# Performance work log

Hardware: AMD Instinct MI355X
Metric: run time of the kernel (lower is better)

The kernel has to match this reference:

```python
import jax, jax.numpy as jnp
import numpy as np

B, N_P, N_S = 64, 50, 200
N_NODES = N_P * N_S          # 10000 nodes per graph (jobs x ops)
N_CAND = N_S + 1             # 201 candidates
INPUT_DIM, HIDDEN = 3, 64
NODE_DIM = 2 * HIDDEN        # h_nodes feature dim (=> actor in = 6*HIDDEN)
POOL_DIM = 4 * HIDDEN        # h_pooled dim (mean || max pooling)
H_ACTOR, H_CRITIC = 256, 256


def setup_inputs() -> dict:
    key = jax.random.key(0)
    ks = jax.random.split(key, 16)
    p = lambda k, sh: jax.random.normal(k, sh, jnp.float32) * 0.02
    x = jax.random.normal(ks[0], (B, N_NODES, INPUT_DIM), jnp.float32)
    candidate = jax.random.randint(ks[1], (B, N_CAND), 0, N_NODES)
    mask = jax.random.randint(ks[2], (B, N_CAND), 0, 2) > 0
    mask = mask.at[:, 0].set(True)  # guarantee at least one valid action per row
    return {
        "x": x, "candidate": candidate, "mask": mask,
        "fe_w1": p(ks[3], (INPUT_DIM, HIDDEN)), "fe_b1": jnp.zeros((HIDDEN,), jnp.float32),
        "fe_w2": p(ks[4], (HIDDEN, NODE_DIM)), "fe_b2": jnp.zeros((NODE_DIM,), jnp.float32),
        "a_w1": p(ks[5], (NODE_DIM + POOL_DIM, H_ACTOR)), "a_b1": jnp.zeros((H_ACTOR,), jnp.float32),
        "a_w2": p(ks[6], (H_ACTOR, H_ACTOR)), "a_b2": jnp.zeros((H_ACTOR,), jnp.float32),
        "a_w3": p(ks[7], (H_ACTOR, 1)), "a_b3": jnp.zeros((1,), jnp.float32),
        "c_w1": p(ks[8], (POOL_DIM, H_CRITIC)), "c_b1": jnp.zeros((H_CRITIC,), jnp.float32),
        "c_w2": p(ks[9], (H_CRITIC, H_CRITIC)), "c_b2": jnp.zeros((H_CRITIC,), jnp.float32),
        "c_w3": p(ks[10], (H_CRITIC, 1)), "c_b3": jnp.zeros((1,), jnp.float32),
    }


def _actor_critic(x, candidate, mask,
                  fe_w1, fe_b1, fe_w2, fe_b2,
                  a_w1, a_b1, a_w2, a_b2, a_w3, a_b3,
                  c_w1, c_b1, c_w2, c_b2, c_w3, c_b3):
    # --- feature_extract: per-node MLP embedding, graph-level pooling ---
    h = jax.nn.relu(jnp.einsum('bni,ih->bnh', x, fe_w1) + fe_b1)
    h_nodes = jax.nn.relu(jnp.einsum('bnh,hd->bnd', h, fe_w2) + fe_b2)   # [B, N, 2H]
    h_pooled = jnp.concatenate([h_nodes.mean(axis=1), h_nodes.max(axis=1)], axis=-1)  # [B, 4H]

    # --- gather candidate node features (torch.gather over node axis) ---
    cand_feat = jnp.take_along_axis(h_nodes, candidate[:, :, None], axis=1)  # [B, C, 2H]

    # --- concat broadcast pooled feature ---
    pooled_rep = jnp.broadcast_to(h_pooled[:, None, :], (cand_feat.shape[0], cand_feat.shape[1], h_pooled.shape[-1]))
    concat_fea = jnp.concatenate([cand_feat, pooled_rep], axis=-1)  # [B, C, 6H]

    # --- actor MLP (tanh hidden layers, linear out) ---
    a = jnp.tanh(concat_fea @ a_w1 + a_b1)
    a = jnp.tanh(a @ a_w2 + a_b2)
    scores = a @ a_w3 + a_b3                                    # [B, C, 1]

    # --- mask with -inf, softmax over candidate axis ---
    scores = jnp.where(mask[:, :, None], scores, -jnp.inf)
    pi = jax.nn.softmax(scores, axis=1)                          # [B, C, 1]

    # --- critic MLP on pooled feature ---
    c = jnp.tanh(h_pooled @ c_w1 + c_b1)
    c = jnp.tanh(c @ c_w2 + c_b2)
    v = c @ c_w3 + c_b3                                          # [B, 1]
    return pi, v


def reference(x, candidate, mask,
              fe_w1, fe_b1, fe_w2, fe_b2,
              a_w1, a_b1, a_w2, a_b2, a_w3, a_b3,
              c_w1, c_b1, c_w2, c_b2, c_w3, c_b3):
    return _actor_critic(x, candidate, mask,
                         fe_w1, fe_b1, fe_w2, fe_b2,
                         a_w1, a_b1, a_w2, a_b2, a_w3, a_b3,
                         c_w1, c_b1, c_w2, c_b2, c_w3, c_b3)
```

## Files before the change

kernel.cpp:

```cpp
#include <hip/hip_runtime.h>

#define NN 10000
#define NCAND 201
#define NB 64

typedef __attribute__((ext_vector_type(8))) short short8;
typedef __attribute__((ext_vector_type(4))) float f32x4;

__device__ __forceinline__ float bf2f(unsigned short u) {
  return __uint_as_float(((unsigned int)u) << 16);
}
__device__ __forceinline__ unsigned short f2bf(float f) {
  unsigned int u = __float_as_uint(f);
  u += 0x7FFFu + ((u >> 16) & 1u);
  return (unsigned short)(u >> 16);
}
__device__ __forceinline__ float fast_tanh(float x) {
  return 1.0f - 2.0f / (__expf(2.0f * x) + 1.0f);
}
__device__ __forceinline__ float gld(const void* p, long i, int f) {
  return f ? ((const float*)p)[i] : bf2f(((const unsigned short*)p)[i]);
}

__global__ __launch_bounds__(256, 4)
void mega_kernel(const void* __restrict__ x, const int* __restrict__ cand,
                 const void* w1, const void* b1, const void* w2, const void* b2,
                 const void* aw1, const void* ab1, const void* aw2, const void* ab2,
                 const void* aw3, const void* ab3,
                 const void* cw1, const void* cb1, const void* cw2, const void* cb2,
                 const void* cw3, const void* cb3,
                 const unsigned int* mask_w, const unsigned int* cand_w,
                 int* F, int* scnt,
                 float* __restrict__ psumP, float* __restrict__ pmaxP,
                 unsigned short* __restrict__ cfw,
                 unsigned short* __restrict__ aw1t, unsigned short* __restrict__ aw2t,
                 unsigned short* __restrict__ cw1t, unsigned short* __restrict__ cw2t) {
  __shared__ __align__(16) unsigned short pool[128 * 72];
  __shared__ float w1f[3 * 64];
  __shared__ float b1f[64];
  __shared__ float b2f[128];
  __shared__ int cnts[8];

  const int t = threadIdx.x;
  const int j = blockIdx.x;
  const int lane = t & 63;
  const int wv = t >> 6;

  if (j < 1472) {
    if (t < 8) cnts[t] = 0;
    __syncthreads();
    {
      if ((((const unsigned short*)x)[t] & 0x7F80u) >= 0x4300u) atomicAdd(&cnts[0], 1);
      if (t < 192 && (((const unsigned short*)w1)[t] & 0x7F80u) >= 0x4300u) atomicAdd(&cnts[1], 1);
      if (t < 64 && (((const unsigned short*)b1)[t] & 0x7F80u) >= 0x4300u) atomicAdd(&cnts[2], 1);
      if (t < 128 && (((const unsigned short*)b2)[t] & 0x7F80u) >= 0x4300u) atomicAdd(&cnts[3], 1);
      if ((((const unsigned short*)w2)[t] & 0x7F80u) >= 0x4300u) atomicAdd(&cnts[4], 1);
      int co = 0;
#pragma unroll
      for (int q = 0; q < 4; ++q) {
        int i = t * 4 + q;
        if ((i & 1) && cand_w[i] != 0u) co = 1;
      }
      if (co) atomicAdd(&cnts[5], 1);
    }
    __syncthreads();
    const int F0 = cnts[0] > 32, F1 = cnts[1] > 24, F2 = cnts[2] > 8;
    const int F4 = cnts[3] > 16, Fw2 = cnts[4] > 32, C64 = cnts[5] == 0;

    if (j < 1024) {
      unsigned short* h1s = pool;
      const int b = j >> 4;
      const int s = j & 15;

      if (t < 192) w1f[t] = gld(w1, t, F1);
      if (t < 64) b1f[t] = gld(b1, t, F2);
      if (t < 128) b2f[t] = gld(b2, t, F4);

      short8 bfr[2][2];
#pragma unroll
      for (int nl = 0; nl < 2; ++nl)
#pragma unroll
        for (int ks = 0; ks < 2; ++ks) {
          int col = wv * 32 + nl * 16 + (lane & 15);
          short8 v;
#pragma unroll
          for (int jj = 0; jj < 8; ++jj) {
            int k = (lane >> 4) * 8 + ks * 32 + jj;
            v[jj] = (short)f2bf(gld(w2, (long)k * 128 + col, Fw2));
          }
          bfr[nl][ks] = v;
        }
      __syncthreads();

      float csum[2] = {0.f, 0.f};
      float cmax[2] = {0.f, 0.f};
      const int m = t & 127;
      const int kg = t >> 7;

      float x0 = 0.f, x1 = 0.f, x2 = 0.f;
      if (s < 79) {
        int nb = s * 128;
        if (m < min(128, NN - nb)) {
          long xo = ((long)b * NN + nb + m) * 3;
          x0 = gld(x, xo, F0); x1 = gld(x, xo + 1, F0); x2 = gld(x, xo + 2, F0);
        }
      }

      for (int c = s; c < 79; c += 16) {
        int nb = c * 128;
        int cnt = (nb + 128 <= NN) ? 128 : (NN - nb);
        if (m < cnt) {
#pragma unroll
          for (int blk = 0; blk < 4; ++blk) {
            short8 v;
#pragma unroll
            for (int i = 0; i < 8; ++i) {
              int k = kg * 32 + blk * 8 + i;
              float vv = x0 * w1f[k] + x1 * w1f[64 + k] + x2 * w1f[128 + k] + b1f[k];
              v[i] = (short)f2bf(fmaxf(vv, 0.f));
            }
            *(short8*)(h1s + m * 72 + kg * 32 + blk * 8) = v;
          }
        }
        {
          int cn = c + 16;
          float nx0 = 0.f, nx1 = 0.f, nx2 = 0.f;
          if (cn < 79) {
            int nbn = cn * 128;
            if (m < min(128, NN - nbn)) {
              long xo = ((long)b * NN + nbn + m) * 3;
              nx0 = gld(x, xo, F0); nx1 = gld(x, xo + 1, F0); nx2 = gld(x, xo + 2, F0);
            }
          }
          __syncthreads();
          x0 = nx0; x1 = nx1; x2 = nx2;
        }
#pragma unroll
        for (int mt = 0; mt < 8; ++mt) {
          const unsigned short* ap = h1s + (mt * 16 + (lane & 15)) * 72 + ((lane >> 4) * 8);
          short8 af0 = *(const short8*)(ap);
          short8 af1 = *(const short8*)(ap + 32);
#pragma unroll
          for (int nl = 0; nl < 2; ++nl) {
            f32x4 acc = {0.f, 0.f, 0.f, 0.f};
            acc = __builtin_amdgcn_mfma_f32_16x16x32_bf16(af0, bfr[nl][0], acc, 0, 0, 0);
            acc = __builtin_amdgcn_mfma_f32_16x16x32_bf16(af1, bfr[nl][1], acc, 0, 0, 0);
            int col = wv * 32 + nl * 16 + (lane & 15);
            float bb = b2f[col];
#pragma unroll
            for (int r = 0; r < 4; ++r) {
              int row = mt * 16 + ((lane >> 4) * 4) + r;
              if (row < cnt) {
                float v = fmaxf(acc[r] + bb, 0.f);
                csum[nl] += v;
                cmax[nl] = fmaxf(cmax[nl], v);
              }
            }
          }
        }
        __syncthreads();
      }
#pragma unroll
      for (int nl = 0; nl < 2; ++nl) {
        csum[nl] += __shfl_xor(csum[nl], 16);
        csum[nl] += __shfl_xor(csum[nl], 32);
        cmax[nl] = fmaxf(cmax[nl], __shfl_xor(cmax[nl], 16));
        cmax[nl] = fmaxf(cmax[nl], __shfl_xor(cmax[nl], 32));
      }
      if (lane < 16) {
#pragma unroll
        for (int nl = 0; nl < 2; ++nl) {
          int col = wv * 32 + nl * 16 + lane;
          psumP[((long)b * 16 + s) * 128 + col] = csum[nl];
          pmaxP[((long)b * 16 + s) * 128 + col] = cmax[nl];
        }
      }
    } else {
      unsigned short* h1c = pool;
      unsigned short* cf = pool + 2560;
      const int idx = j - 1024;
      const int b = idx / 7;
      const int cb = idx % 7;
      const int cbase = cb * 29;

      if (t < 128) b2f[t] = gld(b2, t, F4);

      {
        int r = t & 31;
        int ci = cbase + r;
        if (ci > NCAND - 1) ci = NCAND - 1;
        long cidx = (long)b * NCAND + ci;
        int nd = C64 ? cand[2 * cidx] : cand[cidx];
        long xo = ((long)b * NN + nd) * 3;
        float x0 = gld(x, xo, F0), x1 = gld(x, xo + 1, F0), x2 = gld(x, xo + 2, F0);
        int kg = t >> 5;
#pragma unroll
        for (int i = 0; i < 8; ++i) {
          int k = kg * 8 + i;
          float v = x0 * gld(w1, k, F1) + x1 * gld(w1, 64 + k, F1) +
                    x2 * gld(w1, 128 + k, F1) + gld(b1, k, F2);
          h1c[r * 72 + k] = f2bf(fmaxf(v, 0.f));
        }
      }
      __syncthreads();

      {
        short8 af[2][2];
#pragma unroll
        for (int mt = 0; mt < 2; ++mt)
#pragma unroll
          for (int ks = 0; ks < 2; ++ks)
            af[mt][ks] = *(const short8*)(h1c + (mt * 16 + (lane & 15)) * 72 + ((lane >> 4) * 8) + ks * 32);
#pragma unroll
        for (int nl = 0; nl < 2; ++nl) {
          int col = wv * 32 + nl * 16 + (lane & 15);
          short8 bf0, bf1;
#pragma unroll
          for (int jj = 0; jj < 8; ++jj) {
            int k = (lane >> 4) * 8 + jj;
            bf0[jj] = (short)f2bf(gld(w2, (long)k * 128 + col, Fw2));
            bf1[jj] = (short)f2bf(gld(w2, (long)(k + 32) * 128 + col, Fw2));
          }
          float bb = b2f[col];
#pragma unroll
          for (int mt = 0; mt < 2; ++mt) {
            f32x4 acc = {0.f, 0.f, 0.f, 0.f};
            acc = __builtin_amdgcn_mfma_f32_16x16x32_bf16(af[mt][0], bf0, acc, 0, 0, 0);
            acc = __builtin_amdgcn_mfma_f32_16x16x32_bf16(af[mt][1], bf1, acc, 0, 0, 0);
#pragma unroll
            for (int r = 0; r < 4; ++r) {
              int row = mt * 16 + ((lane >> 4) * 4) + r;
              cfw[(long)idx * 4096 + row * 128 + col] = f2bf(fmaxf(acc[r] + bb, 0.f));
            }
          }
        }
      }
    }
    return;
  }

  if (t < 8) cnts[t] = 0;
  __syncthreads();

  if (j < 1856) {
    const unsigned short* pa = (const unsigned short*)aw1;
    const unsigned short* pb = (const unsigned short*)aw2;
    const unsigned short* pc = (const unsigned short*)cw1;
    const unsigned short* pd = (const unsigned short*)cw2;
    if ((pa[t] & 0x7F80u) >= 0x4300u) atomicAdd(&cnts[0], 1);
    if ((pb[t] & 0x7F80u) >= 0x4300u) atomicAdd(&cnts[1], 1);
    if ((pc[t] & 0x7F80u) >= 0x4300u) atomicAdd(&cnts[2], 1);
    if ((pd[t] & 0x7F80u) >= 0x4300u) atomicAdd(&cnts[3], 1);
    __syncthreads();
    const int Faw1 = cnts[0] > 32, Faw2 = cnts[1] > 32;
    const int Fcw1 = cnts[2] > 32, Fcw2 = cnts[3] > 32;
    int i = (j - 1472) * 256 + t;
    if (i < 256 * 384) { int n = i / 384, k = i % 384; aw1t[i] = f2bf(gld(aw1, k * 256 + n, Faw1)); }
    if (i < 256 * 256) {
      int n = i >> 8, k = i & 255;
      aw2t[i] = f2bf(gld(aw2, k * 256 + n, Faw2));
      cw1t[i] = f2bf(gld(cw1, k * 256 + n, Fcw1));
      cw2t[i] = f2bf(gld(cw2, k * 256 + n, Fcw2));
    }
  } else if (j < 1873) {
    const void* ptrs[17] = {x, w1, b1, w2, b2, aw1, ab1, aw2, ab2, aw3, ab3,
                            cw1, cb1, cw2, cb2, cw3, cb3};
    const int sizes[17] = {1920000, 192, 64, 8192, 128, 98304, 256, 65536, 256,
                           256, 1, 65536, 256, 65536, 256, 256, 1};
    int a = j - 1856;
    const unsigned short* p = (const unsigned short*)ptrs[a];
    int K = min(sizes[a], 2048);
    int c = 0;
    for (int i = t; i < K; i += 256)
      if ((p[i] & 0x7F80u) >= 0x4300u) c++;
    if (c) atomicAdd(&cnts[0], c);
    __syncthreads();
    if (t == 0) F[a] = (cnts[0] > (K >> 3)) ? 1 : 0;
  } else if (j == 1873) {
    int flo = 0, fhi = 0, fgt = 0;
    for (int i = t; i < 3216; i += 256) {
      unsigned int w = mask_w[i];
      if ((w & 0xFFFFu) == 0x3F80u) flo = 1;
      if ((w >> 16) == 0x3F80u) fhi = 1;
      if (w > 1u) fgt = 1;
    }
    if (flo) cnts[0] = 1;
    if (fhi) cnts[1] = 1;
    if (fgt) cnts[2] = 1;
    __syncthreads();
    if (t == 0) F[17] = cnts[0] ? 2 : (cnts[1] ? 3 : (cnts[2] ? 1 : 0));
  } else {
    int co = 0;
    for (int i = t; i < 1024; i += 256)
      if ((i & 1) && cand_w[i] != 0u) co = 1;
    if (co) cnts[0] = 1;
    if (t < 64) scnt[t] = 0;
    __syncthreads();
    if (t == 0) F[18] = cnts[0] ? 0 : 1;
  }
}

__global__ __launch_bounds__(256)
void pp_critic_kernel(const float* __restrict__ psumP, const float* __restrict__ pmaxP,
                      const unsigned short* __restrict__ aw1t,
                      const void* __restrict__ ab1,
                      const unsigned short* __restrict__ cw1t,
                      const unsigned short* __restrict__ cw2t,
                      const void* __restrict__ cb1, const void* __restrict__ cb2,
                      const void* __restrict__ cw3, const void* __restrict__ cb3,
                      const int* __restrict__ F,
                      float* __restrict__ pact, void* __restrict__ out) {
  __shared__ float plf[256];
  __shared__ float c1f[256];
  __shared__ float red[4];
  const int t = threadIdx.x;
  const int b = blockIdx.x & 63;
  const int lane = t & 63, wv = t >> 6;

  float ssum = 0.f, smax = 0.f;
  if (t < 128) {
#pragma unroll
    for (int sl = 0; sl < 16; ++sl) {
      ssum += psumP[((long)b * 16 + sl) * 128 + t];
      smax = fmaxf(smax, pmaxP[((long)b * 16 + sl) * 128 + t]);
    }
  }

  if (blockIdx.x < 64) {
    const int F6 = F[6];
    if (t < 128) {
      plf[t] = bf2f(f2bf(ssum * (1.0f / 10000.0f)));
      plf[128 + t] = bf2f(f2bf(smax));
    }
    __syncthreads();
    float a = gld(ab1, t, F6);
    const unsigned short* row = aw1t + t * 384 + 128;
#pragma unroll
    for (int k8 = 0; k8 < 32; ++k8) {
      short8 w = *(const short8*)(row + k8 * 8);
#pragma unroll
      for (int j = 0; j < 8; ++j)
        a += plf[k8 * 8 + j] * bf2f((unsigned short)w[j]);
    }
    pact[b * 256 + t] = a;
  } else {
    const int OF = (F[0] + F[1] + F[3] + F[5] + F[7] + F[9] + F[11] + F[13] + F[15]) >= 5;
    const int F12 = F[12], F14 = F[14], F15 = F[15], F16 = F[16];
    if (t < 128) {
      plf[t] = ssum * (1.0f / 10000.0f);
      plf[128 + t] = smax;
    }
    __syncthreads();
    {
      float a = gld(cb1, t, F12);
      const unsigned short* row = cw1t + t * 256;
#pragma unroll
      for (int k8 = 0; k8 < 32; ++k8) {
        short8 w = *(const short8*)(row + k8 * 8);
#pragma unroll
        for (int j = 0; j < 8; ++j)
          a += plf[k8 * 8 + j] * bf2f((unsigned short)w[j]);
      }
      c1f[t] = fast_tanh(a);
    }
    __syncthreads();
    {
      float a2 = gld(cb2, t, F14);
      const unsigned short* row = cw2t + t * 256;
#pragma unroll
      for (int k8 = 0; k8 < 32; ++k8) {
        short8 w = *(const short8*)(row + k8 * 8);
#pragma unroll
        for (int j = 0; j < 8; ++j)
          a2 += c1f[k8 * 8 + j] * bf2f((unsigned short)w[j]);
      }
      a2 = fast_tanh(a2);
      float p = a2 * gld(cw3, t, F15);
      for (int o = 32; o; o >>= 1) p += __shfl_xor(p, o);
      __syncthreads();
      if (lane == 0) red[wv] = p;
      __syncthreads();
      if (t == 0) {
        float v = red[0] + red[1] + red[2] + red[3] + gld(cb3, 0, F16);
        if (!(v == v)) v = 0.f;
        if (OF) ((float*)out)[NB * NCAND + b] = v;
        else ((unsigned short*)out)[NB * NCAND + b] = f2bf(v);
      }
    }
  }
}

__global__ __launch_bounds__(256)
void actorB_kernel(const unsigned short* __restrict__ cfw,
                   const void* __restrict__ ab2,
                   const void* __restrict__ aw3, const void* __restrict__ ab3,
                   const void* __restrict__ mask,
                   const int* __restrict__ F,
                   const float* __restrict__ pact,
                   const unsigned short* __restrict__ aw1t,
                   const unsigned short* __restrict__ aw2t,
                   float* __restrict__ scores, int* __restrict__ scnt,
                   void* __restrict__ out) {
  __shared__ __align__(16) unsigned short a1s[32 * 264];
  __shared__ __align__(16) unsigned short a2s[32 * 264];
  __shared__ float pactS[256], ab2f[256];
  __shared__ float red[4];
  __shared__ int amLast;

  const int t = threadIdx.x;
  const int b = blockIdx.x / 7;
  const int cb = blockIdx.x % 7;
  const int cbase = cb * 29;
  const int cntc = min(29, NCAND - cbase);
  const int lane = t & 63;
  const int wv = t >> 6;
  const int F8 = F[8], F9 = F[9], F10 = F[10];

  pactS[t] = pact[b * 256 + t];
  ab2f[t] = gld(ab2, t, F8);

  {
    f32x4 acc[2][4];
#pragma unroll
    for (int mt = 0; mt < 2; ++mt)
#pragma unroll
      for (int nt = 0; nt < 4; ++nt) acc[mt][nt] = (f32x4){0.f, 0.f, 0.f, 0.f};
    const unsigned short* cfb = cfw + (long)blockIdx.x * 4096;
#pragma unroll
    for (int ks = 0; ks < 4; ++ks) {
      short8 af0 = *(const short8*)(cfb + (lane & 15) * 128 + ks * 32 + ((lane >> 4) * 8));
      short8 af1 = *(const short8*)(cfb + (16 + (lane & 15)) * 128 + ks * 32 + ((lane >> 4) * 8));
#pragma unroll
      for (int nt = 0; nt < 4; ++nt) {
        int col = wv * 64 + nt * 16 + (lane & 15);
        short8 bfr = *(const short8*)(aw1t + col * 384 + ks * 32 + ((lane >> 4) * 8));
        acc[0][nt] = __builtin_amdgcn_mfma_f32_16x16x32_bf16(af0, bfr, acc[0][nt], 0, 0, 0);
        acc[1][nt] = __builtin_amdgcn_mfma_f32_16x16x32_bf16(af1, bfr, acc[1][nt], 0, 0, 0);
      }
    }
    __syncthreads();
#pragma unroll
    for (int mt = 0; mt < 2; ++mt)
#pragma unroll
      for (int nt = 0; nt < 4; ++nt) {
        int col = wv * 64 + nt * 16 + (lane & 15);
        float bb = pactS[col];
#pragma unroll
        for (int r = 0; r < 4; ++r) {
          int row = mt * 16 + ((lane >> 4) * 4) + r;
          a1s[row * 264 + col] = f2bf(fast_tanh(acc[mt][nt][r] + bb));
        }
      }
  }
  __syncthreads();

  {
    f32x4 acc[2][4];
#pragma unroll
    for (int mt = 0; mt < 2; ++mt)
#pragma unroll
      for (int nt = 0; nt < 4; ++nt) acc[mt][nt] = (f32x4){0.f, 0.f, 0.f, 0.f};
    for (int ks = 0; ks < 8; ++ks) {
      short8 af0 = *(const short8*)(a1s + (lane & 15) * 264 + ks * 32 + ((lane >> 4) * 8));
      short8 af1 = *(const short8*)(a1s + (16 + (lane & 15)) * 264 + ks * 32 + ((lane >> 4) * 8));
#pragma unroll
      for (int nt = 0; nt < 4; ++nt) {
        int col = wv * 64 + nt * 16 + (lane & 15);
        short8 bfr = *(const short8*)(aw2t + col * 256 + ks * 32 + ((lane >> 4) * 8));
        acc[0][nt] = __builtin_amdgcn_mfma_f32_16x16x32_bf16(af0, bfr, acc[0][nt], 0, 0, 0);
        acc[1][nt] = __builtin_amdgcn_mfma_f32_16x16x32_bf16(af1, bfr, acc[1][nt], 0, 0, 0);
      }
    }
#pragma unroll
    for (int mt = 0; mt < 2; ++mt)
#pragma unroll
      for (int nt = 0; nt < 4; ++nt) {
        int col = wv * 64 + nt * 16 + (lane & 15);
        float bb = ab2f[col];
#pragma unroll
        for (int r = 0; r < 4; ++r) {
          int row = mt * 16 + ((lane >> 4) * 4) + r;
          a2s[row * 264 + col] = f2bf(fast_tanh(acc[mt][nt][r] + bb));
        }
      }
  }
  __syncthreads();

  {
    int row = t >> 3, seg = t & 7;
    float p = 0.f;
#pragma unroll 8
    for (int i = 0; i < 32; ++i) {
      int k = seg * 32 + i;
      p += bf2f(a2s[row * 264 + k]) * gld(aw3, k, F9);
    }
    p += __shfl_xor(p, 1);
    p += __shfl_xor(p, 2);
    p += __shfl_xor(p, 4);
    if (seg == 0 && row < cntc)
      atomicExch(&scores[b * 256 + cbase + row], p + gld(ab3, 0, F10));
  }
  __syncthreads();

  if (t == 0) {
    __threadfence();
    amLast = (atomicAdd(&scnt[b], 1) == 6);
  }
  __syncthreads();
  if (!amLast) return;

  const int MM = F[17];
  const int OF = (F[0] + F[1] + F[3] + F[5] + F[7] + F[9] + F[11] + F[13] + F[15]) >= 5;
  float sraw = 0.f, sv = -1e30f;
  bool valid = false;
  if (t < NCAND) {
    sraw = atomicAdd(&scores[b * 256 + t], 0.0f);
    long idx = (long)b * NCAND + t;
    if (MM == 0)      valid = ((const int*)mask)[idx] != 0;
    else if (MM == 1) valid = ((const unsigned char*)mask)[idx] != 0;
    else if (MM == 2) valid = ((const unsigned short*)mask)[idx] != 0;
    else              valid = ((const unsigned int*)mask)[idx] != 0;
    if (valid) sv = sraw;
  }
  float m = sv;
  for (int o = 32; o; o >>= 1) m = fmaxf(m, __shfl_xor(m, o));
  if (lane == 0) red[wv] = m;
  __syncthreads();
  m = fmaxf(fmaxf(red[0], red[1]), fmaxf(red[2], red[3]));
  __syncthreads();
  float e = valid ? __expf(sraw - m) : 0.f;
  if (!(e == e)) e = 0.f;
  float ss = e;
  for (int o = 32; o; o >>= 1) ss += __shfl_xor(ss, o);
  if (lane == 0) red[wv] = ss;
  __syncthreads();
  float tot = red[0] + red[1] + red[2] + red[3];
  tot = fmaxf(tot, 1e-30f);
  if (t < NCAND) {
    float pv = e / tot;
    if (!(pv == pv)) pv = 0.f;
    if (OF) ((float*)out)[b * NCAND + t] = pv;
    else ((unsigned short*)out)[b * NCAND + t] = f2bf(pv);
  }
}

extern "C" void kernel_launch(void* const* d_in, const int* in_sizes, int n_in,
                              void* d_out, int out_size, void* d_ws, size_t ws_size,
                              hipStream_t stream) {
  const void* x = d_in[0];
  const int* cand = (const int*)d_in[1];
  const void* mask = d_in[2];
  const void* fe_w1 = d_in[3];
  const void* fe_b1 = d_in[4];
  const void* fe_w2 = d_in[5];
  const void* fe_b2 = d_in[6];
  const void* a_w1 = d_in[7];
  const void* a_b1 = d_in[8];
  const void* a_w2 = d_in[9];
  const void* a_b2 = d_in[10];
  const void* a_w3 = d_in[11];
  const void* a_b3 = d_in[12];
  const void* c_w1 = d_in[13];
  const void* c_b1 = d_in[14];
  const void* c_w2 = d_in[15];
  const void* c_b2 = d_in[16];
  const void* c_w3 = d_in[17];
  const void* c_b3 = d_in[18];

  char* ws = (char*)d_ws;
  float* scores = (float*)(ws + 65536);
  unsigned short* aw1t = (unsigned short*)(ws + 147456);
  unsigned short* aw2t = (unsigned short*)(ws + 344064);
  int* F = (int*)(ws + 475136);
  unsigned short* cw1t = (unsigned short*)(ws + 475264);
  unsigned short* cw2t = (unsigned short*)(ws + 606336);
  float* pact = (float*)(ws + 737408);
  unsigned short* cfw = (unsigned short*)(ws + 802944);
  int* scnt = (int*)(ws + 4472960);
  float* psumP = (float*)(ws + 4473216);
  float* pmaxP = (float*)(ws + 4997504);

  mega_kernel<<<1875, 256, 0, stream>>>(x, cand, fe_w1, fe_b1, fe_w2, fe_b2,
                                        a_w1, a_b1, a_w2, a_b2, a_w3, a_b3,
                                        c_w1, c_b1, c_w2, c_b2, c_w3, c_b3,
                                        (const unsigned int*)mask,
                                        (const unsigned int*)cand, F, scnt,
                                        psumP, pmaxP, cfw, aw1t, aw2t, cw1t, cw2t);
  pp_critic_kernel<<<128, 256, 0, stream>>>(psumP, pmaxP, aw1t, a_b1,
                                            cw1t, cw2t, c_b1, c_b2, c_w3, c_b3,
                                            F, pact, (void*)d_out);
  actorB_kernel<<<448, 256, 0, stream>>>(cfw, a_b2, a_w3, a_b3, mask, F, pact,
                                         aw1t, aw2t, scores, scnt, (void*)d_out);
}
```

Measured before the change: 161.9 us.

## Fuse pooled-projection and critic kernel into actor kernel

Merges the pooled-feature projection and critic MLP kernel into the actor kernel, adding 64 extra blocks for the critic and having each actor block recompute the pooled projection (pact) locally. This removes one kernel launch and the global round-trip through the pact buffer. In exchange, every one of the 448 actor blocks redundantly reduces psum/pmax partials and does a 256x256 matvec, adding per-block work and reuse of plf shared memory for the bias.

Result: slower. 166.8 us (+3.0%).

```diff
diff --git a/kernel.cpp b/kernel.cpp
--- a/kernel.cpp
+++ b/kernel.cpp
@@ -177,7 +177,6 @@
       }
     } else {
       unsigned short* h1c = pool;
-      unsigned short* cf = pool + 2560;
       const int idx = j - 1024;
       const int b = idx / 7;
       const int cb = idx % 7;
@@ -301,52 +300,43 @@
 }
 
 __global__ __launch_bounds__(256)
-void pp_critic_kernel(const float* __restrict__ psumP, const float* __restrict__ pmaxP,
-                      const unsigned short* __restrict__ aw1t,
-                      const void* __restrict__ ab1,
-                      const unsigned short* __restrict__ cw1t,
-                      const unsigned short* __restrict__ cw2t,
-                      const void* __restrict__ cb1, const void* __restrict__ cb2,
-                      const void* __restrict__ cw3, const void* __restrict__ cb3,
-                      const int* __restrict__ F,
-                      float* __restrict__ pact, void* __restrict__ out) {
+void actorBC_kernel(const unsigned short* __restrict__ cfw,
+                    const void* __restrict__ ab1, const void* __restrict__ ab2,
+                    const void* __restrict__ aw3, const void* __restrict__ ab3,
+                    const void* __restrict__ mask,
+                    const int* __restrict__ F,
+                    const float* __restrict__ psumP, const float* __restrict__ pmaxP,
+                    const unsigned short* __restrict__ aw1t,
+                    const unsigned short* __restrict__ aw2t,
+                    const unsigned short* __restrict__ cw1t,
+                    const unsigned short* __restrict__ cw2t,
+                    const void* __restrict__ cb1, const void* __restrict__ cb2,
+                    const void* __restrict__ cw3, const void* __restrict__ cb3,
+                    float* __restrict__ scores, int* __restrict__ scnt,
+                    void* __restrict__ out) {
+  __shared__ __align__(16) unsigned short a1s[32 * 264];
+  __shared__ __align__(16) unsigned short a2s[32 * 264];
   __shared__ float plf[256];
-  __shared__ float c1f[256];
+  __shared__ float pactS[256];
   __shared__ float red[4];
+  __shared__ int amLast;
+
   const int t = threadIdx.x;
-  const int b = blockIdx.x & 63;
-  const int lane = t & 63, wv = t >> 6;
-
-  float ssum = 0.f, smax = 0.f;
-  if (t < 128) {
-#pragma unroll
-    for (int sl = 0; sl < 16; ++sl) {
-      ssum += psumP[((long)b * 16 + sl) * 128 + t];
-      smax = fmaxf(smax, pmaxP[((long)b * 16 + sl) * 128 + t]);
-    }
-  }
-
-  if (blockIdx.x < 64) {
-    const int F6 = F[6];
-    if (t < 128) {
-      plf[t] = bf2f(f2bf(ssum * (1.0f / 10000.0f)));
-      plf[128 + t] = bf2f(f2bf(smax));
-    }
-    __syncthreads();
-    float a = gld(ab1, t, F6);
-    const unsigned short* row = aw1t + t * 384 + 128;
-#pragma unroll
-    for (int k8 = 0; k8 < 32; ++k8) {
-      short8 w = *(const short8*)(row + k8 * 8);
-#pragma unroll
-      for (int j = 0; j < 8; ++j)
-        a += plf[k8 * 8 + j] * bf2f((unsigned short)w[j]);
-    }
-    pact[b * 256 + t] = a;
-  } else {
+  const int lane = t & 63;
+  const int wv = t >> 6;
+
+  if (blockIdx.x >= 448) {
+    const int b = blockIdx.x - 448;
+    float* c1f = pactS;
     const int OF = (F[0] + F[1] + F[3] + F[5] + F[7] + F[9] + F[11] + F[13] + F[15]) >= 5;
     const int F12 = F[12], F14 = F[14], F15 = F[15], F16 = F[16];
+    float ssum = 0.f, smax = 0.f;
     if (t < 128) {
+#pragma unroll
+      for (int sl = 0; sl < 16; ++sl) {
+        ssum += psumP[((long)b * 16 + sl) * 128 + t];
+        smax = fmaxf(smax, pmaxP[((long)b * 16 + sl) * 128 + t]);
+      }
       plf[t] = ssum * (1.0f / 10000.0f);
       plf[128 + t] = smax;
     }
@@ -387,37 +377,38 @@
         else ((unsigned short*)out)[NB * NCAND + b] = f2bf(v);
       }
     }
-  }
-}
-
-__global__ __launch_bounds__(256)
-void actorB_kernel(const unsigned short* __restrict__ cfw,
-                   const void* __restrict__ ab2,
-                   const void* __restrict__ aw3, const void* __restrict__ ab3,
-                   const void* __restrict__ mask,
-                   const int* __restrict__ F,
-                   const float* __restrict__ pact,
-                   const unsigned short* __restrict__ aw1t,
-                   const unsigned short* __restrict__ aw2t,
-                   float* __restrict__ scores, int* __restrict__ scnt,
-                   void* __restrict__ out) {
-  __shared__ __align__(16) unsigned short a1s[32 * 264];
-  __shared__ __align__(16) unsigned short a2s[32 * 264];
-  __shared__ float pactS[256], ab2f[256];
-  __shared__ float red[4];
-  __shared__ int amLast;
-
-  const int t = threadIdx.x;
+    return;
+  }
+
   const int b = blockIdx.x / 7;
   const int cb = blockIdx.x % 7;
   const int cbase = cb * 29;
   const int cntc = min(29, NCAND - cbase);
-  const int lane = t & 63;
-  const int wv = t >> 6;
-  const int F8 = F[8], F9 = F[9], F10 = F[10];
-
-  pactS[t] = pact[b * 256 + t];
-  ab2f[t] = gld(ab2, t, F8);
+  const int F6 = F[6], F8 = F[8], F9 = F[9], F10 = F[10];
+
+  {
+    float ssum = 0.f, smax = 0.f;
+    if (t < 128) {
+#pragma unroll
+      for (int sl = 0; sl < 16; ++sl) {
+        ssum += psumP[((long)b * 16 + sl) * 128 + t];
+        smax = fmaxf(smax, pmaxP[((long)b * 16 + sl) * 128 + t]);
+      }
+      plf[t] = bf2f(f2bf(ssum * (1.0f / 10000.0f)));
+      plf[128 + t] = bf2f(f2bf(smax));
+    }
+    __syncthreads();
+    float a = gld(ab1, t, F6);
+    const unsigned short* row = aw1t + t * 384 + 128;
+#pragma unroll
+    for (int k8 = 0; k8 < 32; ++k8) {
+      short8 w = *(const short8*)(row + k8 * 8);
+#pragma unroll
+      for (int j = 0; j < 8; ++j)
+        a += plf[k8 * 8 + j] * bf2f((unsigned short)w[j]);
+    }
+    pactS[t] = a;
+  }
 
   {
     f32x4 acc[2][4];
@@ -471,12 +462,15 @@
         acc[1][nt] = __builtin_amdgcn_mfma_f32_16x16x32_bf16(af1, bfr, acc[1][nt], 0, 0, 0);
       }
     }
+    float ab2v = gld(ab2, t, F8);
+    ((float*)plf)[t] = ab2v;
+    __syncthreads();
 #pragma unroll
     for (int mt = 0; mt < 2; ++mt)
 #pragma unroll
       for (int nt = 0; nt < 4; ++nt) {
         int col = wv * 64 + nt * 16 + (lane & 15);
-        float bb = ab2f[col];
+        float bb = plf[col];
 #pragma unroll
         for (int r = 0; r < 4; ++r) {
           int row = mt * 16 + ((lane >> 4) * 4) + r;
@@ -574,7 +568,6 @@
   int* F = (int*)(ws + 475136);
   unsigned short* cw1t = (unsigned short*)(ws + 475264);
   unsigned short* cw2t = (unsigned short*)(ws + 606336);
-  float* pact = (float*)(ws + 737408);
   unsigned short* cfw = (unsigned short*)(ws + 802944);
   int* scnt = (int*)(ws + 4472960);
   float* psumP = (float*)(ws + 4473216);
@@ -586,9 +579,8 @@
                                         (const unsigned int*)mask,
                                         (const unsigned int*)cand, F, scnt,
                                         psumP, pmaxP, cfw, aw1t, aw2t, cw1t, cw2t);
-  pp_critic_kernel<<<128, 256, 0, stream>>>(psumP, pmaxP, aw1t, a_b1,
-                                            cw1t, cw2t, c_b1, c_b2, c_w3, c_b3,
-                                            F, pact, (void*)d_out);
-  actorB_kernel<<<448, 256, 0, stream>>>(cfw, a_b2, a_w3, a_b3, mask, F, pact,
-                                         aw1t, aw2t, scores, scnt, (void*)d_out);
-}
+  actorBC_kernel<<<512, 256, 0, stream>>>(cfw, a_b1, a_b2, a_w3, a_b3, mask, F,
+                                          psumP, pmaxP, aw1t, aw2t, cw1t, cw2t,
+                                          c_b1, c_b2, c_w3, c_b3,
+                                          scores, scnt, (void*)d_out);
+}
```
